# Kernel tuning notes

Measured on AMD Instinct MI355X. Metric: run time of the kernel, lower is better.

The kernel has to match this reference:

```python
import jax, jax.numpy as jnp
import numpy as np

LEAKY_ALPHA = 0.2  # tf.nn.leaky_relu default


def setup_inputs() -> dict:
    key = jax.random.key(0)
    ks = jax.random.split(key, 8)
    N, F_IN, OUT, E = 100000, 256, 64, 1600000
    x = jax.random.normal(ks[0], (1, N, F_IN), dtype=jnp.float32)
    W = jax.random.normal(ks[1], (F_IN, OUT), dtype=jnp.float32) * 0.05
    a1 = jax.random.normal(ks[2], (OUT, 1), dtype=jnp.float32) * 0.1
    b1 = jnp.zeros((1,), dtype=jnp.float32)
    a2 = jax.random.normal(ks[3], (OUT, 1), dtype=jnp.float32) * 0.1
    b2 = jnp.zeros((1,), dtype=jnp.float32)
    out_bias = jnp.zeros((OUT,), dtype=jnp.float32)
    edge_src = jax.random.randint(ks[4], (E,), 0, N, dtype=jnp.int32)
    edge_dst = jax.random.randint(ks[5], (E,), 0, N, dtype=jnp.int32)
    return {"x": x, "W": W, "a1": a1, "b1": b1, "a2": a2, "b2": b2,
            "out_bias": out_bias, "edge_src": edge_src, "edge_dst": edge_dst,
            "nb_nodes": N}


def reference(x, W, a1, b1, a2, b2, out_bias, edge_src, edge_dst, nb_nodes):
    N = int(nb_nodes)
    h = jnp.einsum('nf,fo->no', x[0], W)          # [N, out_sz] projected features
    f1 = (h @ a1 + b1)[:, 0]                       # [N] per-node src score
    f2 = (h @ a2 + b2)[:, 0]                       # [N] per-node dst score
    # edge logits: f1[src] + f2[dst], leaky relu
    e = jax.nn.leaky_relu(f1[edge_src] + f2[edge_dst], negative_slope=LEAKY_ALPHA)
    # row-wise sparse softmax over edges grouped by src
    m = jax.ops.segment_max(e, edge_src, num_segments=N)
    m = jnp.where(jnp.isfinite(m), m, 0.0)
    ex = jnp.exp(e - m[edge_src])
    denom = jax.ops.segment_sum(ex, edge_src, num_segments=N)
    coefs = ex / denom[edge_src]                   # [E]
    # spmm: aggregate neighbor features
    vals = jax.ops.segment_sum(coefs[:, None] * h[edge_dst], edge_src, num_segments=N)
    ret = jax.nn.elu(vals + out_bias)              # bias_add + elu act
    return ret[None]                               # [1, N, out_sz]
```

## Files before the change

### kernel.cpp

```cpp
#include <hip/hip_runtime.h>
#include <math.h>

#define F_IN 256
#define OUT  64
#define LEAKY 0.2f
#define BSH  9
#define BSZ  512
#define CAP  12288

typedef __attribute__((ext_vector_type(4))) float f32x4;
typedef __attribute__((ext_vector_type(8))) __bf16 bf16x8;
typedef __attribute__((ext_vector_type(4))) unsigned int u32x4;

__device__ __forceinline__ unsigned cvt_pk_bf16(float lo, float hi) {
    unsigned r;
    asm volatile("v_cvt_pk_bf16_f32 %0, %1, %2" : "=v"(r) : "v"(lo), "v"(hi));
    return r;
}

__device__ __forceinline__ void gload_lds16(const float* g, float* l) {
    __builtin_amdgcn_global_load_lds((const __attribute__((address_space(1))) void*)g,
                                     (__attribute__((address_space(3))) void*)l, 16, 0, 0);
}

__global__ __launch_bounds__(256) void fused_part_gemm_kernel(
    const float* __restrict__ x, const float* __restrict__ W,
    const float* __restrict__ a1, const float* __restrict__ b1,
    const float* __restrict__ a2, const float* __restrict__ b2,
    unsigned short* __restrict__ h2, float* __restrict__ f1, float* __restrict__ f2,
    const int* __restrict__ esrc, const int* __restrict__ edst,
    int* __restrict__ gcur, unsigned* __restrict__ ebkt,
    int N, int E, int nPart, int gemmBlocks)
{
    __shared__ __align__(16) unsigned int Wt[64 * 128];
    __shared__ __align__(16) float xs[4][2][1024];

    const int bid = blockIdx.x;
    const int t   = threadIdx.x;
    const int r   = bid % 3;

    if (r == 2) {
        int c = bid / 3;
        if (c >= nPart) return;
        int* hist = (int*)&xs[0][0][0];
        int* run  = hist + 256;
        int* off  = hist + 512;
        hist[t] = 0; off[t] = 0;
        __syncthreads();
        const int e0 = c * 4096;
        int ss[16], dd[16], bb[16];
#pragma unroll
        for (int k = 0; k < 4; ++k) {
            int i = e0 + k * 1024 + t * 4;
            if (i + 4 <= E) {
                int4 s4 = *(const int4*)&esrc[i];
                int4 d4 = *(const int4*)&edst[i];
                ss[k * 4 + 0] = s4.x; ss[k * 4 + 1] = s4.y;
                ss[k * 4 + 2] = s4.z; ss[k * 4 + 3] = s4.w;
                dd[k * 4 + 0] = d4.x; dd[k * 4 + 1] = d4.y;
                dd[k * 4 + 2] = d4.z; dd[k * 4 + 3] = d4.w;
#pragma unroll
                for (int q = 0; q < 4; ++q) {
                    bb[k * 4 + q] = ss[k * 4 + q] >> BSH;
                    atomicAdd(&hist[bb[k * 4 + q]], 1);
                }
            } else {
#pragma unroll
                for (int q = 0; q < 4; ++q) {
                    int e = i + q;
                    if (e < E) {
                        ss[k * 4 + q] = esrc[e];
                        dd[k * 4 + q] = edst[e];
                        bb[k * 4 + q] = ss[k * 4 + q] >> BSH;
                        atomicAdd(&hist[bb[k * 4 + q]], 1);
                    } else bb[k * 4 + q] = -1;
                }
            }
        }
        __syncthreads();
        if (hist[t] > 0) run[t] = t * CAP + atomicAdd(&gcur[t], hist[t]);
        __syncthreads();
#pragma unroll
        for (int k = 0; k < 16; ++k) {
            if (bb[k] >= 0) {
                int l = atomicAdd(&off[bb[k]], 1);
                ebkt[run[bb[k]] + l] = (unsigned)dd[k] |
                                       ((unsigned)(ss[k] & (BSZ - 1)) << 17);
            }
        }
        return;
    }

    const int g    = (bid / 3) * 2 + r;
    if (g >= gemmBlocks) return;
    const int wave = t >> 6;
    const int lane = t & 63;
    const int rowB = g * 128;

    for (int p = t; p < 64 * 32; p += 256) {
        int c = p & 63, gg = p >> 6;
        float f[8];
#pragma unroll
        for (int j = 0; j < 8; ++j) f[j] = W[(gg * 8 + j) * 64 + c];
        u32x4 d;
        d.x = cvt_pk_bf16(f[0], f[1]);
        d.y = cvt_pk_bf16(f[2], f[3]);
        d.z = cvt_pk_bf16(f[4], f[5]);
        d.w = cvt_pk_bf16(f[6], f[7]);
        int gs = gg ^ (c & 7);
        *(u32x4*)&Wt[c * 128 + gs * 4] = d;
    }

    auto stage = [&](int buf, int kc) {
#pragma unroll
        for (int i = 0; i < 4; ++i) {
            int lrow = i * 8 + (lane >> 3);
            int gg   = lane & 7;
            int srow = rowB + wave * 32 + lrow; if (srow > N - 1) srow = N - 1;
            int gsw  = gg ^ (lrow & 7);
            const float* src = x + (size_t)srow * F_IN + kc + gsw * 4;
            gload_lds16(src, &xs[wave][buf][i * 256]);
        }
    };

    f32x4 acc[2][4];
#pragma unroll
    for (int m = 0; m < 2; ++m)
#pragma unroll
        for (int n = 0; n < 4; ++n) acc[m][n] = (f32x4){0.f, 0.f, 0.f, 0.f};

    stage(0, 0);
    __syncthreads();

#pragma unroll 1
    for (int ks = 0; ks < 8; ++ks) {
        const int cur = ks & 1;
        if (ks < 7) {
            stage(cur ^ 1, (ks + 1) * 32);
            asm volatile("s_waitcnt vmcnt(4)" ::: "memory");
        } else {
            asm volatile("s_waitcnt vmcnt(0)" ::: "memory");
        }
        __builtin_amdgcn_sched_barrier(0);

        bf16x8 bfrag[4];
#pragma unroll
        for (int ns = 0; ns < 4; ++ns) {
            int c = ns * 16 + (lane & 15);
            int G = ks * 4 + (lane >> 4);
            u32x4 bw = *(u32x4*)&Wt[c * 128 + ((G ^ (c & 7)) << 2)];
            bfrag[ns] = __builtin_bit_cast(bf16x8, bw);
        }
#pragma unroll
        for (int ms = 0; ms < 2; ++ms) {
            int lrow = ms * 16 + (lane & 15);
            int g0   = (lane >> 4) * 2;
            float4 xa = *(float4*)&xs[wave][cur][lrow * 32 + (((g0 + 0) ^ (lrow & 7)) << 2)];
            float4 xb = *(float4*)&xs[wave][cur][lrow * 32 + (((g0 + 1) ^ (lrow & 7)) << 2)];
            u32x4 ad;
            ad.x = cvt_pk_bf16(xa.x, xa.y);
            ad.y = cvt_pk_bf16(xa.z, xa.w);
            ad.z = cvt_pk_bf16(xb.x, xb.y);
            ad.w = cvt_pk_bf16(xb.z, xb.w);
            bf16x8 afrag = __builtin_bit_cast(bf16x8, ad);
#pragma unroll
            for (int ns = 0; ns < 4; ++ns)
                acc[ms][ns] = __builtin_amdgcn_mfma_f32_16x16x32_bf16(afrag, bfrag[ns],
                                                                      acc[ms][ns], 0, 0, 0);
        }
    }

    float A1v[4], A2v[4];
#pragma unroll
    for (int ns = 0; ns < 4; ++ns) {
        A1v[ns] = a1[ns * 16 + (lane & 15)];
        A2v[ns] = a2[ns * 16 + (lane & 15)];
    }
    float B1 = b1[0], B2 = b2[0];
#pragma unroll
    for (int ms = 0; ms < 2; ++ms) {
#pragma unroll
        for (int rr = 0; rr < 4; ++rr) {
            int grow = rowB + wave * 32 + ms * 16 + ((lane >> 4) << 2) + rr;
            float s1 = 0.f, s2 = 0.f;
#pragma unroll
            for (int ns = 0; ns < 4; ++ns) {
                float v = acc[ms][ns][rr];
                if (grow < N)
                    h2[(size_t)grow * OUT + ns * 16 + (lane & 15)] =
                        (unsigned short)(cvt_pk_bf16(v, v) & 0xffffu);
                s1 += v * A1v[ns];
                s2 += v * A2v[ns];
            }
#pragma unroll
            for (int off = 1; off < 16; off <<= 1) {
                s1 += __shfl_xor(s1, off);
                s2 += __shfl_xor(s2, off);
            }
            if ((lane & 15) == 0 && grow < N) { f1[grow] = s1 + B1; f2[grow] = s2 + B2; }
        }
    }
}

__global__ __launch_bounds__(256) void csr_build_kernel(
    const unsigned* __restrict__ ebkt, const int* __restrict__ gcur,
    int* __restrict__ counts, int* __restrict__ row_start,
    int* __restrict__ csr4, int N)
{
    __shared__ int cnt[BSZ];
    __shared__ int cur[BSZ];
    __shared__ int sc[2][BSZ];
    const int b = blockIdx.x;
    const int t = threadIdx.x;

    cnt[t] = 0; cnt[t + 256] = 0;
    __syncthreads();

    const int e0 = b * CAP;
    const int e1 = e0 + gcur[b];
    for (int i = e0 + t; i < e1; i += 256)
        atomicAdd(&cnt[ebkt[i] >> 17], 1);
    __syncthreads();

    sc[0][t] = cnt[t]; sc[0][t + 256] = cnt[t + 256];
    __syncthreads();
    int srcb = 0;
    for (int d = 1; d < BSZ; d <<= 1) {
        int dstb = srcb ^ 1;
        int i0 = t, i1 = t + 256;
        sc[dstb][i0] = sc[srcb][i0] + (i0 >= d ? sc[srcb][i0 - d] : 0);
        sc[dstb][i1] = sc[srcb][i1] + (i1 >= d ? sc[srcb][i1 - d] : 0);
        __syncthreads();
        srcb = dstb;
    }

    const int nodeBase = b << BSH;
#pragma unroll
    for (int j = 0; j < 2; ++j) {
        int i = t + j * 256;
        int excl = sc[srcb][i] - cnt[i];
        cur[i] = excl;
        int gn = nodeBase + i;
        if (gn < N) {
            row_start[gn] = e0 + excl;
            counts[gn]    = cnt[i];
        }
    }
    __syncthreads();

    for (int i = e0 + t; i < e1; i += 256) {
        unsigned w = ebkt[i];
        int ls = w >> 17;
        int pos = e0 + atomicAdd(&cur[ls], 1);
        csr4[pos] = (int)(w & 0x1FFFFu);
    }
}

__global__ __launch_bounds__(256) void aggregate_kernel(
    const unsigned short* __restrict__ h2, const float* __restrict__ f1,
    const float* __restrict__ f2,
    const int* __restrict__ row_start, const int* __restrict__ counts,
    const int* __restrict__ csr4, const float* __restrict__ out_bias,
    float* __restrict__ out, int N)
{
    const int t    = threadIdx.x;
    const int lane = t & 63;
    const int gl   = lane & 15;
    const int gb   = lane & 48;
    const int gw   = blockIdx.x * 16 + ((t >> 6) << 2) + (lane >> 4);
    if (gw >= N) return;

    const int base  = row_start[gw];
    const int deg   = counts[gw];
    const float f1n = f1[gw];

    float den = 0.f;
    float a0 = 0.f, a1f = 0.f, a2f = 0.f, a3f = 0.f;

    for (int c0 = 0; c0 < deg; c0 += 16) {
        int  idx   = c0 + gl;
        bool valid = idx < deg;
        int   d = valid ? csr4[base + idx] : 0;
        float e = f1n + f2[d];
        e = (e > 0.f) ? e : LEAKY * e;
        float p = valid ? __expf(e) : 0.f;
        den += p;

        unsigned pack = ((unsigned)d << 15) | (cvt_pk_bf16(p, p) & 0x7FFFu);

        int lim = deg - c0; if (lim > 16) lim = 16;
        int j = 0;
        for (; j + 2 <= lim; j += 2) {
            unsigned pk0 = __shfl((int)pack, gb + j);
            unsigned pk1 = __shfl((int)pack, gb + j + 1);
            uint2 u0 = *(const uint2*)&h2[((pk0 >> 15) << 6) + (gl << 2)];
            uint2 u1 = *(const uint2*)&h2[((pk1 >> 15) << 6) + (gl << 2)];
            float p0 = __builtin_bit_cast(float, (pk0 & 0x7FFFu) << 16);
            float p1 = __builtin_bit_cast(float, (pk1 & 0x7FFFu) << 16);
            a0  += p0 * __builtin_bit_cast(float, u0.x << 16)
                 + p1 * __builtin_bit_cast(float, u1.x << 16);
            a1f += p0 * __builtin_bit_cast(float, u0.x & 0xFFFF0000u)
                 + p1 * __builtin_bit_cast(float, u1.x & 0xFFFF0000u);
            a2f += p0 * __builtin_bit_cast(float, u0.y << 16)
                 + p1 * __builtin_bit_cast(float, u1.y << 16);
            a3f += p0 * __builtin_bit_cast(float, u0.y & 0xFFFF0000u)
                 + p1 * __builtin_bit_cast(float, u1.y & 0xFFFF0000u);
        }
        if (j < lim) {
            unsigned pk = __shfl((int)pack, gb + j);
            uint2 u = *(const uint2*)&h2[((pk >> 15) << 6) + (gl << 2)];
            float pp = __builtin_bit_cast(float, (pk & 0x7FFFu) << 16);
            a0  += pp * __builtin_bit_cast(float, u.x << 16);
            a1f += pp * __builtin_bit_cast(float, u.x & 0xFFFF0000u);
            a2f += pp * __builtin_bit_cast(float, u.y << 16);
            a3f += pp * __builtin_bit_cast(float, u.y & 0xFFFF0000u);
        }
    }

    den += __shfl_xor(den, 1);
    den += __shfl_xor(den, 2);
    den += __shfl_xor(den, 4);
    den += __shfl_xor(den, 8);

    float rd = (deg > 0) ? (1.f / den) : 0.f;
    float4 bias = *(const float4*)&out_bias[gl << 2];
    float v0 = a0  * rd + bias.x;
    float v1 = a1f * rd + bias.y;
    float v2 = a2f * rd + bias.z;
    float v3 = a3f * rd + bias.w;
    v0 = (v0 > 0.f) ? v0 : (__expf(v0) - 1.f);
    v1 = (v1 > 0.f) ? v1 : (__expf(v1) - 1.f);
    v2 = (v2 > 0.f) ? v2 : (__expf(v2) - 1.f);
    v3 = (v3 > 0.f) ? v3 : (__expf(v3) - 1.f);
    float4 res = {v0, v1, v2, v3};
    *(float4*)&out[((unsigned)gw << 6) + (gl << 2)] = res;
}

extern "C" void kernel_launch(void* const* d_in, const int* in_sizes, int n_in,
                              void* d_out, int out_size, void* d_ws, size_t ws_size,
                              hipStream_t stream)
{
    const float* x        = (const float*)d_in[0];
    const float* W        = (const float*)d_in[1];
    const float* a1       = (const float*)d_in[2];
    const float* b1       = (const float*)d_in[3];
    const float* a2       = (const float*)d_in[4];
    const float* b2       = (const float*)d_in[5];
    const float* out_bias = (const float*)d_in[6];
    const int*   esrc     = (const int*)d_in[7];
    const int*   edst     = (const int*)d_in[8];
    const int N = in_sizes[0] / F_IN;
    const int E = in_sizes[7];
    float* out = (float*)d_out;

    char* wsp = (char*)d_ws;
    size_t off = 0;
    auto alloc = [&](size_t bytes) -> void* {
        void* p = wsp + off;
        off = (off + bytes + 255) & ~(size_t)255;
        return p;
    };
    const int nbk = (N + BSZ - 1) >> BSH;

    unsigned short* h2 = (unsigned short*)alloc((size_t)N * OUT * sizeof(unsigned short));
    float* f1          = (float*)alloc((size_t)N * sizeof(float));
    float* f2          = (float*)alloc((size_t)N * sizeof(float));
    int*   counts      = (int*)alloc((size_t)N * sizeof(int));
    int*   row_start   = (int*)alloc((size_t)N * sizeof(int));
    int*   gcur        = (int*)alloc(256 * sizeof(int));
    unsigned* ebkt     = (unsigned*)alloc((size_t)nbk * CAP * sizeof(unsigned));
    int*   csr4        = (int*)alloc((size_t)nbk * CAP * sizeof(int));

    const int nPart      = (E + 4095) / 4096;
    const int gemmBlocks = (N + 127) / 128;
    int nGroup = (gemmBlocks + 1) / 2;
    if (nPart > nGroup) nGroup = nPart;

    hipMemsetAsync(gcur, 0, 256 * sizeof(int), stream);

    fused_part_gemm_kernel<<<nGroup * 3, 256, 0, stream>>>(
        x, W, a1, b1, a2, b2, h2, f1, f2, esrc, edst, gcur, ebkt, N, E, nPart, gemmBlocks);
    csr_build_kernel<<<nbk, 256, 0, stream>>>(ebkt, gcur, counts, row_start, csr4, N);
    aggregate_kernel<<<(N + 15) / 16, 256, 0, stream>>>(h2, f1, f2, row_start, counts, csr4,
                                                        out_bias, out, N);
}
```

Measured before the change: 107.1 us.

## Replace global bucket atomics with per-partition local scan and run table

The partition phase no longer reserves space in global buckets with atomicAdd on a shared cursor array. Each edge partition now does a local prefix scan over its bucket histogram, writes its edges bucket-sorted into its own contiguous slice, and records per-bucket run starts and counts. The CSR build then walks the run table for its bucket across all partitions, and the memset of the global cursor is dropped. This removes global atomic contention, but each CSR block now reads many small, strided runs with serial per-thread inner loops, which could hurt memory coalescing.

```diff
diff --git a/kernel.cpp b/kernel.cpp
--- a/kernel.cpp
+++ b/kernel.cpp
@@ -7,6 +7,7 @@
 #define BSH  9
 #define BSZ  512
 #define CAP  12288
+#define EPB  4096
 
 typedef __attribute__((ext_vector_type(4))) float f32x4;
 typedef __attribute__((ext_vector_type(8))) __bf16 bf16x8;
@@ -29,7 +30,7 @@
     const float* __restrict__ a2, const float* __restrict__ b2,
     unsigned short* __restrict__ h2, float* __restrict__ f1, float* __restrict__ f2,
     const int* __restrict__ esrc, const int* __restrict__ edst,
-    int* __restrict__ gcur, unsigned* __restrict__ ebkt,
+    int* __restrict__ runstart, int* __restrict__ cntmat, unsigned* __restrict__ ebkt,
     int N, int E, int nPart, int gemmBlocks)
 {
     __shared__ __align__(16) unsigned int Wt[64 * 128];
@@ -43,11 +44,13 @@
         int c = bid / 3;
         if (c >= nPart) return;
         int* hist = (int*)&xs[0][0][0];
-        int* run  = hist + 256;
-        int* off  = hist + 512;
+        int* off  = hist + 256;
+        int* run  = hist + 512;
+        int* sc0  = hist + 768;
+        int* sc1  = hist + 1024;
         hist[t] = 0; off[t] = 0;
         __syncthreads();
-        const int e0 = c * 4096;
+        const int e0 = c * EPB;
         int ss[16], dd[16], bb[16];
 #pragma unroll
         for (int k = 0; k < 4; ++k) {
@@ -78,14 +81,24 @@
             }
         }
         __syncthreads();
-        if (hist[t] > 0) run[t] = t * CAP + atomicAdd(&gcur[t], hist[t]);
+        sc0[t] = hist[t];
+        __syncthreads();
+        int* s = sc0; int* dsts = sc1;
+        for (int d = 1; d < 256; d <<= 1) {
+            dsts[t] = s[t] + (t >= d ? s[t - d] : 0);
+            __syncthreads();
+            int* tmp = s; s = dsts; dsts = tmp;
+        }
+        run[t] = s[t] - hist[t];
+        runstart[c * 256 + t] = s[t] - hist[t];
+        cntmat [c * 256 + t] = hist[t];
         __syncthreads();
 #pragma unroll
         for (int k = 0; k < 16; ++k) {
             if (bb[k] >= 0) {
                 int l = atomicAdd(&off[bb[k]], 1);
-                ebkt[run[bb[k]] + l] = (unsigned)dd[k] |
-                                       ((unsigned)(ss[k] & (BSZ - 1)) << 17);
+                ebkt[e0 + run[bb[k]] + l] = (unsigned)dd[k] |
+                                            ((unsigned)(ss[k] & (BSZ - 1)) << 17);
             }
         }
         return;
@@ -203,9 +216,10 @@
 }
 
 __global__ __launch_bounds__(256) void csr_build_kernel(
-    const unsigned* __restrict__ ebkt, const int* __restrict__ gcur,
+    const unsigned* __restrict__ ebkt, const int* __restrict__ runstart,
+    const int* __restrict__ cntmat,
     int* __restrict__ counts, int* __restrict__ row_start,
-    int* __restrict__ csr4, int N)
+    int* __restrict__ csr4, int N, int nPart)
 {
     __shared__ int cnt[BSZ];
     __shared__ int cur[BSZ];
@@ -216,10 +230,12 @@
     cnt[t] = 0; cnt[t + 256] = 0;
     __syncthreads();
 
-    const int e0 = b * CAP;
-    const int e1 = e0 + gcur[b];
-    for (int i = e0 + t; i < e1; i += 256)
-        atomicAdd(&cnt[ebkt[i] >> 17], 1);
+    for (int c = t; c < nPart; c += 256) {
+        int base = c * EPB + runstart[c * 256 + b];
+        int n    = cntmat[c * 256 + b];
+        for (int i = 0; i < n; ++i)
+            atomicAdd(&cnt[ebkt[base + i] >> 17], 1);
+    }
     __syncthreads();
 
     sc[0][t] = cnt[t]; sc[0][t + 256] = cnt[t + 256];
@@ -235,6 +251,7 @@
     }
 
     const int nodeBase = b << BSH;
+    const int e0out    = b * CAP;
 #pragma unroll
     for (int j = 0; j < 2; ++j) {
         int i = t + j * 256;
@@ -242,17 +259,21 @@
         cur[i] = excl;
         int gn = nodeBase + i;
         if (gn < N) {
-            row_start[gn] = e0 + excl;
+            row_start[gn] = e0out + excl;
             counts[gn]    = cnt[i];
         }
     }
     __syncthreads();
 
-    for (int i = e0 + t; i < e1; i += 256) {
-        unsigned w = ebkt[i];
-        int ls = w >> 17;
-        int pos = e0 + atomicAdd(&cur[ls], 1);
-        csr4[pos] = (int)(w & 0x1FFFFu);
+    for (int c = t; c < nPart; c += 256) {
+        int base = c * EPB + runstart[c * 256 + b];
+        int n    = cntmat[c * 256 + b];
+        for (int i = 0; i < n; ++i) {
+            unsigned w = ebkt[base + i];
+            int ls = w >> 17;
+            int pos = e0out + atomicAdd(&cur[ls], 1);
+            csr4[pos] = (int)(w & 0x1FFFFu);
+        }
     }
 }
 
@@ -360,27 +381,28 @@
         off = (off + bytes + 255) & ~(size_t)255;
         return p;
     };
-    const int nbk = (N + BSZ - 1) >> BSH;
+    const int nbk   = (N + BSZ - 1) >> BSH;
+    const int nPart = (E + EPB - 1) / EPB;
 
     unsigned short* h2 = (unsigned short*)alloc((size_t)N * OUT * sizeof(unsigned short));
     float* f1          = (float*)alloc((size_t)N * sizeof(float));
     float* f2          = (float*)alloc((size_t)N * sizeof(float));
     int*   counts      = (int*)alloc((size_t)N * sizeof(int));
     int*   row_start   = (int*)alloc((size_t)N * sizeof(int));
-    int*   gcur        = (int*)alloc(256 * sizeof(int));
-    unsigned* ebkt     = (unsigned*)alloc((size_t)nbk * CAP * sizeof(unsigned));
+    int*   runstart    = (int*)alloc((size_t)nPart * 256 * sizeof(int));
+    int*   cntmat      = (int*)alloc((size_t)nPart * 256 * sizeof(int));
+    unsigned* ebkt     = (unsigned*)alloc((size_t)nPart * EPB * sizeof(unsigned));
     int*   csr4        = (int*)alloc((size_t)nbk * CAP * sizeof(int));
 
-    const int nPart      = (E + 4095) / 4096;
     const int gemmBlocks = (N + 127) / 128;
     int nGroup = (gemmBlocks + 1) / 2;
     if (nPart > nGroup) nGroup = nPart;
 
-    hipMemsetAsync(gcur, 0, 256 * sizeof(int), stream);
-
     fused_part_gemm_kernel<<<nGroup * 3, 256, 0, stream>>>(
-        x, W, a1, b1, a2, b2, h2, f1, f2, esrc, edst, gcur, ebkt, N, E, nPart, gemmBlocks);
-    csr_build_kernel<<<nbk, 256, 0, stream>>>(ebkt, gcur, counts, row_start, csr4, N);
+        x, W, a1, b1, a2, b2, h2, f1, f2, esrc, edst, runstart, cntmat, ebkt,
+        N, E, nPart, gemmBlocks);
+    csr_build_kernel<<<nbk, 256, 0, stream>>>(ebkt, runstart, cntmat, counts, row_start,
+                                              csr4, N, nPart);
     aggregate_kernel<<<(N + 15) / 16, 256, 0, stream>>>(h2, f1, f2, row_start, counts, csr4,
                                                         out_bias, out, N);
 }
```

New measurement: 100.1 us. 1.07x faster.
